# Optimization experiments

Hardware: AMD Instinct MI355X
Metric: run time of the kernel (lower is better)

The kernel has to match this reference:

```python
import jax, jax.numpy as jnp
import numpy as np

U, B, I, D, L = 50000, 20000, 100000, 64, 2
E_UB, E_UI, E_BI = 800000, 1000000, 800000
E_BIAGG, E_UIAGG = 800000, 1000000
UPS_UB = UPS_UI = UPS_BI = 0.1
XI = jnp.array([1.0 / 3, 1.0 / 3, 1.0 / 3], dtype=jnp.float32)  # layer coefs (len L+1)
OMEGA, G1, G2, TAU, LAM1, LAM2 = 0.5, 0.5, 0.5, 0.25, 0.04, 1e-5
BATCH = 2048


def l2norm(x, axis=-1):
    n = jnp.linalg.norm(x, axis=axis, keepdims=True)
    return x / jnp.maximum(n, 1e-12)


def spmm(rows, cols, vals, x, n):
    # sparse [n, m] @ dense [m, D] via gather + segment-sum over COO entries
    return jax.ops.segment_sum(vals[:, None] * x[cols], rows, num_segments=n)


def graph_propagate(rows, cols, vals, A, Bf, noise, ups, xi):
    n = A.shape[0] + Bf.shape[0]
    feats = jnp.concatenate([A, Bf], axis=0)
    alls = [feats]
    for l in range(L):
        feats = spmm(rows, cols, vals, feats, n)
        feats = feats + jnp.sign(feats) * l2norm(noise[l]) * ups  # noise injection
        alls.append(l2norm(feats, axis=1))
    out = jnp.sum(jnp.stack(alls, axis=1) * xi[None, :, None], axis=1)  # weighted layer sum [n, D]
    return out[: A.shape[0]], out[A.shape[0] :]


def graph_aggregate(rows, cols, vals, x, noise, ups, n):
    agg = spmm(rows, cols, vals, x, n)
    return agg + jnp.sign(agg) * l2norm(noise) * ups


def cl_loss(pos, aug):
    pos = l2norm(pos, 1)
    aug = l2norm(aug, 1)
    pos_score = jnp.exp(jnp.sum(pos * aug, axis=1) / TAU)
    ttl = jnp.sum(jnp.exp(pos @ aug.T / TAU), axis=1)
    return -jnp.mean(jnp.log(pos_score / ttl))


def dcbr_forward(users_feature, bundles_feature, items_feature,
                 ub_rows, ub_cols, ub_vals, ui_rows, ui_cols, ui_vals,
                 bi_rows, bi_cols, bi_vals, biagg_rows, biagg_cols, biagg_vals,
                 uiagg_rows, uiagg_cols, uiagg_vals,
                 noise_UB, noise_UI, noise_BI, noise_agg_BI, noise_agg_UI,
                 users, bundles):
    UB_u, UB_b = graph_propagate(ub_rows, ub_cols, ub_vals, users_feature, bundles_feature, noise_UB, UPS_UB, XI)
    UI_u, UI_i = graph_propagate(ui_rows, ui_cols, ui_vals, users_feature, items_feature, noise_UI, UPS_UI, XI)
    UI_b = graph_aggregate(biagg_rows, biagg_cols, biagg_vals, UI_i, noise_agg_BI, UPS_BI, B)
    BI_b, BI_i = graph_propagate(bi_rows, bi_cols, bi_vals, bundles_feature, items_feature, noise_BI, UPS_BI, XI)
    BI_u = graph_aggregate(uiagg_rows, uiagg_cols, uiagg_vals, BI_i, noise_agg_UI, UPS_UI, U)
    users_rep = OMEGA * UI_u + (1 - OMEGA) * BI_u
    bundles_rep = OMEGA * UI_b + (1 - OMEGA) * BI_b
    u_emb = users_rep[users]          # [batch, 1, D] -> broadcasts over negatives
    b_emb = bundles_rep[bundles]      # [batch, 2, D]
    pred = jnp.sum(u_emb * b_emb, axis=2)  # [batch, 2]
    pos, neg = pred[:, :1], pred[:, 1:]
    reg = jnp.sum(users_feature ** 2) + jnp.sum(bundles_feature ** 2) + jnp.sum(items_feature ** 2)
    bpr = -jnp.mean(jax.nn.log_sigmoid(pos - neg)) + LAM2 * reg
    u0, b0 = users[:, 0], bundles[:, 0]
    ub_u, ui_us, bi_us = UB_u[u0], UI_u[u0], BI_u[u0]
    ub_bb, ui_bb, bi_bb = UB_b[b0], UI_b[b0], BI_b[b0]
    u_inter = cl_loss(ub_u, ui_us) + cl_loss(ub_u, bi_us) + cl_loss(ui_us, bi_us)
    b_inter = cl_loss(ub_bb, ui_bb) + cl_loss(ub_bb, bi_bb) + cl_loss(ui_bb, bi_bb)
    u_intra = cl_loss(ub_u, ub_u) + cl_loss(ui_us, ui_us) + cl_loss(bi_us, bi_us)
    b_intra = cl_loss(ub_bb, ub_bb) + cl_loss(ui_bb, ui_bb) + cl_loss(bi_bb, bi_bb)
    cl = LAM1 * (G1 * (u_inter + b_inter) + G2 * (u_intra + b_intra))
    return bpr, cl


def setup_inputs():
    key = jax.random.key(0)
    k = jax.random.split(key, 16)

    def prop_edges(kk, nA, nB, e):
        k1, k2, k3 = jax.random.split(kk, 3)
        a = jax.random.randint(k1, (e,), 0, nA, dtype=jnp.int32)
        b = jax.random.randint(k2, (e,), 0, nB, dtype=jnp.int32) + nA
        v = jax.random.uniform(k3, (e,), jnp.float32, 0.01, 0.2)  # degree-normalized weights
        return jnp.concatenate([a, b]), jnp.concatenate([b, a]), jnp.concatenate([v, v])

    def agg_edges(kk, nA, nB, e):
        k1, k2, k3 = jax.random.split(kk, 3)
        return (jax.random.randint(k1, (e,), 0, nA, dtype=jnp.int32),
                jax.random.randint(k2, (e,), 0, nB, dtype=jnp.int32),
                jax.random.uniform(k3, (e,), jnp.float32, 0.01, 0.2))

    ub_rows, ub_cols, ub_vals = prop_edges(k[0], U, B, E_UB)
    ui_rows, ui_cols, ui_vals = prop_edges(k[1], U, I, E_UI)
    bi_rows, bi_cols, bi_vals = prop_edges(k[2], B, I, E_BI)
    biagg_rows, biagg_cols, biagg_vals = agg_edges(k[3], B, I, E_BIAGG)
    uiagg_rows, uiagg_cols, uiagg_vals = agg_edges(k[4], U, I, E_UIAGG)
    s = 0.02  # xavier-normal-ish scale
    return {
        'users_feature': jax.random.normal(k[5], (U, D), jnp.float32) * s,
        'bundles_feature': jax.random.normal(k[6], (B, D), jnp.float32) * s,
        'items_feature': jax.random.normal(k[7], (I, D), jnp.float32) * s,
        'ub_rows': ub_rows, 'ub_cols': ub_cols, 'ub_vals': ub_vals,
        'ui_rows': ui_rows, 'ui_cols': ui_cols, 'ui_vals': ui_vals,
        'bi_rows': bi_rows, 'bi_cols': bi_cols, 'bi_vals': bi_vals,
        'biagg_rows': biagg_rows, 'biagg_cols': biagg_cols, 'biagg_vals': biagg_vals,
        'uiagg_rows': uiagg_rows, 'uiagg_cols': uiagg_cols, 'uiagg_vals': uiagg_vals,
        'noise_UB': jax.random.uniform(k[8], (L, U + B, D), jnp.float32),
        'noise_UI': jax.random.uniform(k[9], (L, U + I, D), jnp.float32),
        'noise_BI': jax.random.uniform(k[10], (L, B + I, D), jnp.float32),
        'noise_agg_BI': jax.random.uniform(k[11], (B, D), jnp.float32),
        'noise_agg_UI': jax.random.uniform(k[12], (U, D), jnp.float32),
        'users': jax.random.randint(k[13], (BATCH, 1), 0, U, dtype=jnp.int32),
        'bundles': jax.random.randint(k[14], (BATCH, 2), 0, B, dtype=jnp.int32),
    }


def reference(users_feature, bundles_feature, items_feature,
              ub_rows, ub_cols, ub_vals, ui_rows, ui_cols, ui_vals,
              bi_rows, bi_cols, bi_vals, biagg_rows, biagg_cols, biagg_vals,
              uiagg_rows, uiagg_cols, uiagg_vals,
              noise_UB, noise_UI, noise_BI, noise_agg_BI, noise_agg_UI,
              users, bundles):
    return dcbr_forward(users_feature, bundles_feature, items_feature,
                        ub_rows, ub_cols, ub_vals, ui_rows, ui_cols, ui_vals,
                        bi_rows, bi_cols, bi_vals, biagg_rows, biagg_cols, biagg_vals,
                        uiagg_rows, uiagg_cols, uiagg_vals,
                        noise_UB, noise_UI, noise_BI, noise_agg_BI, noise_agg_UI,
                        users, bundles)
```

## Files before the change

### kernel.cpp

```cpp
#include <hip/hip_runtime.h>
#include <cmath>
#include <climits>

#define DD 64

namespace {

constexpr int U_N = 50000, B_N = 20000, I_N = 100000;
constexpr int BATCH = 2048;

constexpr int N1 = 340000, N2 = 70000;
constexpr int SHIFT1 = 10, SHIFT2 = 8;
constexpr int NB1 = (N1 + (1 << SHIFT1) - 1) >> SHIFT1;
constexpr int NB2 = (N2 + (1 << SHIFT2) - 1) >> SHIFT2;

typedef __attribute__((ext_vector_type(8))) short short8;
typedef __attribute__((ext_vector_type(4))) float floatx4;
typedef __attribute__((ext_vector_type(2))) float f32x2;

__device__ __forceinline__ float wave_sum(float v) {
#pragma unroll
  for (int off = 32; off > 0; off >>= 1) v += __shfl_xor(v, off);
  return v;
}

__device__ __forceinline__ float wave_sum16(float v) {
#pragma unroll
  for (int off = 1; off < 16; off <<= 1) v += __shfl_xor(v, off);
  return v;
}

__device__ __forceinline__ unsigned short f2bf(float f) {
  unsigned u = __float_as_uint(f);
  unsigned r = (u + 0x7FFFu + ((u >> 16) & 1u)) >> 16;
  return (unsigned short)r;
}

__device__ __forceinline__ float sgn(float x) {
  return (x > 0.f) ? 1.f : ((x < 0.f) ? -1.f : 0.f);
}

__global__ void k_tobf16(const float* __restrict__ x, unsigned short* __restrict__ o, int n4) {
  int i = blockIdx.x * 256 + threadIdx.x;
  if (i >= n4) return;
  float4 v = ((const float4*)x)[i];
  uint2 p;
  p.x = (unsigned)f2bf(v.x) | ((unsigned)f2bf(v.y) << 16);
  p.y = (unsigned)f2bf(v.z) | ((unsigned)f2bf(v.w) << 16);
  ((uint2*)o)[i] = p;
}

__global__ __launch_bounds__(512) void k_bhist(const int* __restrict__ rows, int nnz,
                                               int row_off, int shift,
                                               const unsigned char* __restrict__ flags,
                                               int* __restrict__ bcnt) {
  __shared__ int h[512];
  int t = threadIdx.x;
  h[t] = 0;
  __syncthreads();
  int tile0 = blockIdx.x * 8192;
#pragma unroll
  for (int i = 0; i < 16; ++i) {
    int e = tile0 + i * 512 + t;
    if (e < nnz) {
      int r = rows[e] + row_off;
      if (!flags || flags[r]) atomicAdd(&h[r >> shift], 1);
    }
  }
  __syncthreads();
  if (h[t]) atomicAdd(&bcnt[t], h[t]);
}

__global__ void k_bucket_scan(const int* __restrict__ bcnt, int nb, int* __restrict__ bbase,
                              int* __restrict__ bcur, int* __restrict__ rowptr_end) {
  int t = threadIdx.x;
  int lane = t & 63, w = t >> 6;
  int v = (t < nb) ? bcnt[t] : 0;
  int inc = v;
#pragma unroll
  for (int off = 1; off < 64; off <<= 1) {
    int y = __shfl_up(inc, off);
    if (lane >= off) inc += y;
  }
  __shared__ int wsum[8];
  if (lane == 63) wsum[w] = inc;
  __syncthreads();
  int wadd = 0;
  for (int i = 0; i < w; ++i) wadd += wsum[i];
  inc += wadd;
  if (t < nb) { bbase[t] = inc - v; bcur[t] = inc - v; }
  if (t == 511) { bbase[nb] = inc; *rowptr_end = inc; }
}

__global__ __launch_bounds__(512) void k_binscatter(const int* __restrict__ rows,
                                                    const int* __restrict__ cols,
                                                    const float* __restrict__ vals, int nnz,
                                                    int row_off, int shift,
                                                    int nAth, int offA, int offB,
                                                    const unsigned char* __restrict__ flags,
                                                    int* __restrict__ bcur,
                                                    int2* __restrict__ ebin_cv) {
  __shared__ int cnt[512];
  __shared__ int gbase[512];
  int t = threadIdx.x;
  int tile0 = blockIdx.x * 8192;
  cnt[t] = 0;
  __syncthreads();
  int r[16], rank[16];
#pragma unroll
  for (int i = 0; i < 16; ++i) {
    int e = tile0 + i * 512 + t;
    rank[i] = -1;
    if (e < nnz) {
      r[i] = rows[e] + row_off;
      if (!flags || flags[r[i]]) rank[i] = atomicAdd(&cnt[r[i] >> shift], 1);
    }
  }
  __syncthreads();
  int c = cnt[t];
  if (c > 0) gbase[t] = atomicAdd(&bcur[t], c);
  __syncthreads();
  int mask = (1 << shift) - 1;
#pragma unroll
  for (int i = 0; i < 16; ++i) {
    int e = tile0 + i * 512 + t;
    if (rank[i] >= 0) {
      int pos = gbase[r[i] >> shift] + rank[i];
      int col = cols[e];
      int gcol = (col < nAth) ? col + offA : col + offB;
      ebin_cv[pos] = make_int2(((r[i] & mask) << 20) | gcol, __float_as_int(vals[e]));
    }
  }
}

__global__ __launch_bounds__(1024) void k_place(const int* __restrict__ bbase, int shift,
                                                int nrows, const int2* __restrict__ ebin_cv,
                                                int* __restrict__ rowptr,
                                                int2* __restrict__ epack) {
  int b = blockIdx.x;
  int bsize = 1 << shift;
  int row0 = b << shift;
  int t = threadIdx.x;
  __shared__ int rcnt[1024];
  __shared__ int wsum[16];
  int ebase = bbase[b], eend = bbase[b + 1];
  if (t < bsize) rcnt[t] = 0;
  __syncthreads();
  for (int e = ebase + t; e < eend; e += 1024)
    atomicAdd(&rcnt[ebin_cv[e].x >> 20], 1);
  __syncthreads();
  int v = (t < bsize) ? rcnt[t] : 0;
  int inc = v;
  int lane = t & 63, w = t >> 6;
#pragma unroll
  for (int off = 1; off < 64; off <<= 1) {
    int y = __shfl_up(inc, off);
    if (lane >= off) inc += y;
  }
  if (lane == 63) wsum[w] = inc;
  __syncthreads();
  int wadd = 0;
  for (int i = 0; i < w; ++i) wadd += wsum[i];
  inc += wadd;
  int excl = inc - v;
  int nr = nrows - row0;
  if (nr > bsize) nr = bsize;
  if (t < nr) rowptr[row0 + t] = ebase + excl;
  __syncthreads();
  if (t < bsize) rcnt[t] = excl;
  __syncthreads();
  for (int e = ebase + t; e < eend; e += 1024) {
    int2 cv = ebin_cv[e];
    int pos = ebase + atomicAdd(&rcnt[cv.x >> 20], 1);
    epack[pos] = make_int2(cv.x & 0xFFFFF, cv.y);
  }
}

__global__ void k_spmm1(const int* __restrict__ rowptr, const int2* __restrict__ epack,
                        const uint2* __restrict__ xg, const float* __restrict__ noise,
                        uint2* __restrict__ s2g, int n, int nAth, int offA, int offB) {
  long long t = (long long)blockIdx.x * 256 + threadIdx.x;
  int row = (int)(t >> 6), lane = (int)(t & 63);
  if (row >= n) return;
  int q = lane >> 4, c = lane & 15;
  unsigned cb = (unsigned)c << 3;
  int s = rowptr[row], e = rowptr[row + 1];
  int em1 = e - 1;
  f32x2 a0[4], a1[4];
#pragma unroll
  for (int j = 0; j < 4; ++j) { a0[j] = (f32x2){0.f, 0.f}; a1[j] = (f32x2){0.f, 0.f}; }
  for (int kk = s; kk < e; kk += 16) {
#pragma unroll
    for (int j = 0; j < 4; ++j) {
      int i = kk + 4 * j + q;
      int ic = min(i, em1);
      int2 ed = epack[ic];
      float v = (i <= em1) ? __int_as_float(ed.y) : 0.f;
      uint2 d = *(const uint2*)((const char*)xg + (((unsigned)ed.x << 7) | cb));
      f32x2 lo = {__uint_as_float(d.x << 16), __uint_as_float(d.x & 0xffff0000u)};
      f32x2 hi = {__uint_as_float(d.y << 16), __uint_as_float(d.y & 0xffff0000u)};
      f32x2 vv = {v, v};
      a0[j] = __builtin_elementwise_fma(lo, vv, a0[j]);
      a1[j] = __builtin_elementwise_fma(hi, vv, a1[j]);
    }
  }
  f32x2 g0 = (a0[0] + a0[1]) + (a0[2] + a0[3]);
  f32x2 g1 = (a1[0] + a1[1]) + (a1[2] + a1[3]);
  float4 g = {g0.x, g0.y, g1.x, g1.y};
  g.x += __shfl_xor(g.x, 16); g.y += __shfl_xor(g.y, 16);
  g.z += __shfl_xor(g.z, 16); g.w += __shfl_xor(g.w, 16);
  g.x += __shfl_xor(g.x, 32); g.y += __shfl_xor(g.y, 32);
  g.z += __shfl_xor(g.z, 32); g.w += __shfl_xor(g.w, 32);
  float4 nz = ((const float4*)(noise + (size_t)row * DD))[c];
  float nn = wave_sum16(nz.x * nz.x + nz.y * nz.y + nz.z * nz.z + nz.w * nz.w) * 0.25f;
  float nf = 0.1f / fmaxf(sqrtf(nn), 1e-12f);
  if (lane < 16) {
    float4 fv;
    fv.x = g.x + sgn(g.x) * nz.x * nf;
    fv.y = g.y + sgn(g.y) * nz.y * nf;
    fv.z = g.z + sgn(g.z) * nz.z * nf;
    fv.w = g.w + sgn(g.w) * nz.w * nf;
    uint2 o;
    o.x = (unsigned)f2bf(fv.x) | ((unsigned)f2bf(fv.y) << 16);
    o.y = (unsigned)f2bf(fv.z) | ((unsigned)f2bf(fv.w) << 16);
    int grow = (row < nAth) ? row + offA : row + offB;
    s2g[grow * 16 + c] = o;
  }
}

__global__ void k_spmm2(const int* __restrict__ rowptr, const int2* __restrict__ epack,
                        const uint2* __restrict__ s2g, const uint2* __restrict__ xg,
                        const float* __restrict__ noise, float* __restrict__ outp,
                        const int* __restrict__ ids, int row_add, int row0, int nw,
                        int nAth, int offA, int offB) {
  long long t = (long long)blockIdx.x * 256 + threadIdx.x;
  int w = (int)(t >> 6), lane = (int)(t & 63);
  if (w >= nw) return;
  int row = ids ? (ids[w] + row_add) : (row0 + w);
  int q = lane >> 4, c = lane & 15;
  unsigned cb = (unsigned)c << 3;
  int s = rowptr[row], e = rowptr[row + 1];
  int em1 = e - 1;
  f32x2 a0[4], a1[4];
#pragma unroll
  for (int j = 0; j < 4; ++j) { a0[j] = (f32x2){0.f, 0.f}; a1[j] = (f32x2){0.f, 0.f}; }
  for (int kk = s; kk < e; kk += 16) {
#pragma unroll
    for (int j = 0; j < 4; ++j) {
      int i = kk + 4 * j + q;
      int ic = min(i, em1);
      int2 ed = epack[ic];
      float v = (i <= em1) ? __int_as_float(ed.y) : 0.f;
      uint2 d = *(const uint2*)((const char*)s2g + (((unsigned)ed.x << 7) | cb));
      f32x2 lo = {__uint_as_float(d.x << 16), __uint_as_float(d.x & 0xffff0000u)};
      f32x2 hi = {__uint_as_float(d.y << 16), __uint_as_float(d.y & 0xffff0000u)};
      f32x2 vv = {v, v};
      a0[j] = __builtin_elementwise_fma(lo, vv, a0[j]);
      a1[j] = __builtin_elementwise_fma(hi, vv, a1[j]);
    }
  }
  f32x2 g0 = (a0[0] + a0[1]) + (a0[2] + a0[3]);
  f32x2 g1 = (a1[0] + a1[1]) + (a1[2] + a1[3]);
  float4 g = {g0.x, g0.y, g1.x, g1.y};
  g.x += __shfl_xor(g.x, 16); g.y += __shfl_xor(g.y, 16);
  g.z += __shfl_xor(g.z, 16); g.w += __shfl_xor(g.w, 16);
  g.x += __shfl_xor(g.x, 32); g.y += __shfl_xor(g.y, 32);
  g.z += __shfl_xor(g.z, 32); g.w += __shfl_xor(g.w, 32);
  float4 nz = ((const float4*)(noise + (size_t)row * DD))[c];
  float nn = wave_sum16(nz.x * nz.x + nz.y * nz.y + nz.z * nz.z + nz.w * nz.w) * 0.25f;
  float nf = 0.1f / fmaxf(sqrtf(nn), 1e-12f);
  float4 fv;
  fv.x = g.x + sgn(g.x) * nz.x * nf;
  fv.y = g.y + sgn(g.y) * nz.y * nf;
  fv.z = g.z + sgn(g.z) * nz.z * nf;
  fv.w = g.w + sgn(g.w) * nz.w * nf;
  float fn2 = wave_sum16(fv.x * fv.x + fv.y * fv.y + fv.z * fv.z + fv.w * fv.w) * 0.25f;
  float inv2 = (1.f / 3.f) / fmaxf(sqrtf(fn2), 1e-12f);
  int grow = (row < nAth) ? row + offA : row + offB;
  uint2 s1p = s2g[grow * 16 + c];
  float4 s1;
  s1.x = __uint_as_float(s1p.x << 16);
  s1.y = __uint_as_float(s1p.x & 0xffff0000u);
  s1.z = __uint_as_float(s1p.y << 16);
  s1.w = __uint_as_float(s1p.y & 0xffff0000u);
  float fn1 = wave_sum16(s1.x * s1.x + s1.y * s1.y + s1.z * s1.z + s1.w * s1.w) * 0.25f;
  float inv1 = (1.f / 3.f) / fmaxf(sqrtf(fn1), 1e-12f);
  uint2 x0p = xg[grow * 16 + c];
  float4 x0;
  x0.x = __uint_as_float(x0p.x << 16);
  x0.y = __uint_as_float(x0p.x & 0xffff0000u);
  x0.z = __uint_as_float(x0p.y << 16);
  x0.w = __uint_as_float(x0p.y & 0xffff0000u);
  if (lane < 16) {
    float4 o;
    o.x = x0.x * (1.f / 3.f) + s1.x * inv1 + fv.x * inv2;
    o.y = x0.y * (1.f / 3.f) + s1.y * inv1 + fv.y * inv2;
    o.z = x0.z * (1.f / 3.f) + s1.z * inv1 + fv.z * inv2;
    o.w = x0.w * (1.f / 3.f) + s1.w * inv1 + fv.w * inv2;
    ((float4*)(outp + (size_t)w * DD))[c] = o;
  }
}

__global__ void k_agg_s(const int* __restrict__ rowptr, const int2* __restrict__ epack,
                        const float* __restrict__ x, const float* __restrict__ noise,
                        const int* __restrict__ ids, int nids, float* __restrict__ out) {
  long long t = (long long)blockIdx.x * 256 + threadIdx.x;
  int w = (int)(t >> 6), lane = (int)(t & 63);
  if (w >= nids) return;
  int row = ids[w];
  int q = lane >> 4, c = lane & 15;
  int s = rowptr[row], e = rowptr[row + 1];
  int em1 = e - 1;
  float4 a0 = {0.f, 0.f, 0.f, 0.f}, a1 = {0.f, 0.f, 0.f, 0.f};
  for (int kk = s; kk < e; kk += 8) {
    int i0 = kk + q, i1 = kk + 4 + q;
    int2 e0 = epack[min(i0, em1)];
    int2 e1 = epack[min(i1, em1)];
    float4 x0 = ((const float4*)(x + (size_t)e0.x * DD))[c];
    float4 x1 = ((const float4*)(x + (size_t)e1.x * DD))[c];
    float v0 = (i0 <= em1) ? __int_as_float(e0.y) : 0.f;
    float v1 = (i1 <= em1) ? __int_as_float(e1.y) : 0.f;
    a0.x = fmaf(v0, x0.x, a0.x); a0.y = fmaf(v0, x0.y, a0.y);
    a0.z = fmaf(v0, x0.z, a0.z); a0.w = fmaf(v0, x0.w, a0.w);
    a1.x = fmaf(v1, x1.x, a1.x); a1.y = fmaf(v1, x1.y, a1.y);
    a1.z = fmaf(v1, x1.z, a1.z); a1.w = fmaf(v1, x1.w, a1.w);
  }
  float4 g;
  g.x = a0.x + a1.x; g.y = a0.y + a1.y; g.z = a0.z + a1.z; g.w = a0.w + a1.w;
  g.x += __shfl_xor(g.x, 16); g.y += __shfl_xor(g.y, 16);
  g.z += __shfl_xor(g.z, 16); g.w += __shfl_xor(g.w, 16);
  g.x += __shfl_xor(g.x, 32); g.y += __shfl_xor(g.y, 32);
  g.z += __shfl_xor(g.z, 32); g.w += __shfl_xor(g.w, 32);
  float4 nz = ((const float4*)(noise + (size_t)row * DD))[c];
  float nn = wave_sum16(nz.x * nz.x + nz.y * nz.y + nz.z * nz.z + nz.w * nz.w) * 0.25f;
  float nf = 0.1f / fmaxf(sqrtf(nn), 1e-12f);
  if (lane < 16) {
    float4 fv;
    fv.x = g.x + sgn(g.x) * nz.x * nf;
    fv.y = g.y + sgn(g.y) * nz.y * nf;
    fv.z = g.z + sgn(g.z) * nz.z * nf;
    fv.w = g.w + sgn(g.w) * nz.w * nf;
    ((float4*)(out + (size_t)w * DD))[c] = fv;
  }
}

__global__ void k_flag(const int* __restrict__ users, const int* __restrict__ bundles,
                       unsigned char* __restrict__ flags) {
  int t = blockIdx.x * 256 + threadIdx.x;
  if (t < BATCH) flags[20000 + users[t]] = 1;
  if (t < 2 * BATCH) flags[bundles[t]] = 1;
}

__global__ void k_bpr(const float* __restrict__ o_UIuS, const float* __restrict__ biuS,
                      const float* __restrict__ uibS, const float* __restrict__ o_BIbS,
                      float* __restrict__ bpr_terms) {
  long long t = (long long)blockIdx.x * 256 + threadIdx.x;
  int w = (int)(t >> 6);
  int lane = (int)(t & 63);
  if (w >= BATCH) return;
  float ur = 0.5f * (o_UIuS[(size_t)w * DD + lane] + biuS[(size_t)w * DD + lane]);
  float br0 = 0.5f * (uibS[(size_t)(2 * w) * DD + lane] + o_BIbS[(size_t)(2 * w) * DD + lane]);
  float br1 = 0.5f * (uibS[(size_t)(2 * w + 1) * DD + lane] +
                      o_BIbS[(size_t)(2 * w + 1) * DD + lane]);
  float pos = wave_sum(ur * br0);
  float neg = wave_sum(ur * br1);
  if (lane == 0) {
    float x = pos - neg;
    float loss = (x > 0.f) ? log1pf(expf(-x)) : (-x + log1pf(expf(x)));
    bpr_terms[w] = loss;
  }
}

__global__ void k_sumsq_p(const float* __restrict__ x, int n4, float* __restrict__ partials) {
  float s = 0.f;
  for (int i = blockIdx.x * 256 + threadIdx.x; i < n4; i += gridDim.x * 256) {
    float4 v = ((const float4*)x)[i];
    s += v.x * v.x + v.y * v.y + v.z * v.z + v.w * v.w;
  }
  s = wave_sum(s);
  __shared__ float part[4];
  if ((threadIdx.x & 63) == 0) part[threadIdx.x >> 6] = s;
  __syncthreads();
  if (threadIdx.x == 0) partials[blockIdx.x] = part[0] + part[1] + part[2] + part[3];
}

__global__ void k_gather(const float* __restrict__ o_UBS, const float* __restrict__ o_UIuS,
                         const float* __restrict__ o_BIbS, const float* __restrict__ uibS,
                         const float* __restrict__ biuS, float* __restrict__ P,
                         unsigned short* __restrict__ Pb) {
  long long t = (long long)blockIdx.x * 256 + threadIdx.x;
  int w = (int)(t >> 6);
  int lane = (int)(t & 63);
  if (w >= 6 * BATCH) return;
  int k = w / BATCH, b = w % BATCH;
  const float* src;
  if (k == 0)      src = o_UBS + (size_t)b * DD;
  else if (k == 1) src = o_UIuS + (size_t)b * DD;
  else if (k == 2) src = biuS + (size_t)b * DD;
  else if (k == 3) src = o_UBS + (size_t)(2048 + 2 * b) * DD;
  else if (k == 4) src = uibS + (size_t)(2 * b) * DD;
  else             src = o_BIbS + (size_t)(2 * b) * DD;
  float v = src[lane];
  float n2 = wave_sum(v * v);
  float inv = 1.f / fmaxf(sqrtf(n2), 1e-12f);
  float pv = v * inv;
  P[(size_t)w * DD + lane] = pv;
  Pb[(size_t)w * DD + lane] = f2bf(pv);
}

__global__ void k_clpair_mfma(const unsigned short* __restrict__ Pb,
                              float* __restrict__ ttl) {
  const int pairX[12] = {0, 0, 1, 0, 1, 2, 3, 3, 4, 3, 4, 5};
  const int pairY[12] = {1, 2, 2, 0, 1, 2, 4, 5, 5, 3, 4, 5};
  int wid = threadIdx.x >> 6;
  int lane = threadIdx.x & 63;
  int wtile = blockIdx.x * 4 + wid;
  int p = wtile >> 8;
  int rest = wtile & 255;
  int it = rest >> 3, jc = rest & 7;
  const unsigned short* X = Pb + (size_t)pairX[p] * BATCH * DD;
  const unsigned short* Y = Pb + (size_t)pairY[p] * BATCH * DD;
  int r = lane & 15, q = lane >> 4;
  short8 A[2][4];
#pragma unroll
  for (int kh = 0; kh < 2; ++kh)
#pragma unroll
    for (int ii = 0; ii < 4; ++ii)
      A[kh][ii] = *(const short8*)(X + (size_t)(it * 64 + ii * 16 + r) * DD + kh * 32 + q * 8);
  float rs[4][4];
#pragma unroll
  for (int ii = 0; ii < 4; ++ii)
#pragma unroll
    for (int g = 0; g < 4; ++g) rs[ii][g] = 0.f;
  for (int jn = 0; jn < 4; ++jn) {
    int j0 = jc * 256 + jn * 64;
    floatx4 acc[4][4];
#pragma unroll
    for (int ii = 0; ii < 4; ++ii)
#pragma unroll
      for (int jj = 0; jj < 4; ++jj) acc[ii][jj] = (floatx4){0.f, 0.f, 0.f, 0.f};
#pragma unroll
    for (int kh = 0; kh < 2; ++kh) {
      short8 Bf[4];
#pragma unroll
      for (int jj = 0; jj < 4; ++jj)
        Bf[jj] = *(const short8*)(Y + (size_t)(j0 + jj * 16 + r) * DD + kh * 32 + q * 8);
#pragma unroll
      for (int ii = 0; ii < 4; ++ii)
#pragma unroll
        for (int jj = 0; jj < 4; ++jj)
          acc[ii][jj] = __builtin_amdgcn_mfma_f32_16x16x32_bf16(A[kh][ii], Bf[jj],
                                                                acc[ii][jj], 0, 0, 0);
    }
#pragma unroll
    for (int ii = 0; ii < 4; ++ii)
#pragma unroll
      for (int jj = 0; jj < 4; ++jj)
#pragma unroll
        for (int g = 0; g < 4; ++g) rs[ii][g] += __expf(4.0f * acc[ii][jj][g]);
  }
#pragma unroll
  for (int off = 1; off < 16; off <<= 1)
#pragma unroll
    for (int ii = 0; ii < 4; ++ii)
#pragma unroll
      for (int g = 0; g < 4; ++g) rs[ii][g] += __shfl_xor(rs[ii][g], off);
  if (r == 0) {
#pragma unroll
    for (int ii = 0; ii < 4; ++ii)
#pragma unroll
      for (int g = 0; g < 4; ++g)
        unsafeAtomicAdd(&ttl[(size_t)p * BATCH + it * 64 + ii * 16 + q * 4 + g],
                        rs[ii][g]);
  }
}

__global__ void k_cldiag(const float* __restrict__ P, float* __restrict__ ttl) {
  const int pairX[12] = {0, 0, 1, 0, 1, 2, 3, 3, 4, 3, 4, 5};
  const int pairY[12] = {1, 2, 2, 0, 1, 2, 4, 5, 5, 3, 4, 5};
  long long t = (long long)blockIdx.x * 256 + threadIdx.x;
  int w = (int)(t >> 6);
  int lane = (int)(t & 63);
  if (w >= 12 * BATCH) return;
  int p = w / BATCH, i = w % BATCH;
  float xv = P[((size_t)pairX[p] * BATCH + i) * DD + lane];
  float yv = P[((size_t)pairY[p] * BATCH + i) * DD + lane];
  float d = wave_sum(xv * yv);
  if (lane == 0) ttl[(size_t)p * BATCH + i] = logf(ttl[(size_t)p * BATCH + i]) - d * 4.0f;
}

__global__ void k_finalred(const float* __restrict__ bpr_terms,
                           const float* __restrict__ cl_terms,
                           const float* __restrict__ partials,
                           float* __restrict__ out) {
  int t = threadIdx.x;
  float bpr = 0.f, reg = 0.f, inter = 0.f, intra = 0.f;
  for (int i = t; i < BATCH; i += 1024) bpr += bpr_terms[i];
  for (int i = t; i < 768; i += 1024) reg += partials[i];
  for (int i = t; i < 12 * BATCH; i += 1024) {
    int p = i >> 11;
    float v = cl_terms[i];
    if ((p % 6) < 3) inter += v; else intra += v;
  }
  bpr = wave_sum(bpr); reg = wave_sum(reg);
  inter = wave_sum(inter); intra = wave_sum(intra);
  __shared__ float sb[16], sr[16], si[16], sx[16];
  int w = t >> 6, lane = t & 63;
  if (lane == 0) { sb[w] = bpr; sr[w] = reg; si[w] = inter; sx[w] = intra; }
  __syncthreads();
  if (t == 0) {
    float Bs = 0, Rs = 0, Is = 0, Xs = 0;
    for (int i = 0; i < 16; ++i) { Bs += sb[i]; Rs += sr[i]; Is += si[i]; Xs += sx[i]; }
    out[0] = Bs / (float)BATCH + 1e-5f * Rs;
    out[1] = 0.04f * (0.5f * Is + 0.5f * Xs) / (float)BATCH;
  }
}

}

extern "C" void kernel_launch(void* const* d_in, const int* in_sizes, int n_in,
                              void* d_out, int out_size, void* d_ws, size_t ws_size,
                              hipStream_t stream) {
  const float* usersF = (const float*)d_in[0];
  const float* bundlesF = (const float*)d_in[1];
  const float* itemsF = (const float*)d_in[2];
  const int* ub_rows = (const int*)d_in[3];
  const int* ub_cols = (const int*)d_in[4];
  const float* ub_vals = (const float*)d_in[5];
  const int* ui_rows = (const int*)d_in[6];
  const int* ui_cols = (const int*)d_in[7];
  const float* ui_vals = (const float*)d_in[8];
  const int* bi_rows = (const int*)d_in[9];
  const int* bi_cols = (const int*)d_in[10];
  const float* bi_vals = (const float*)d_in[11];
  const int* biagg_rows = (const int*)d_in[12];
  const int* biagg_cols = (const int*)d_in[13];
  const float* biagg_vals = (const float*)d_in[14];
  const int* uiagg_rows = (const int*)d_in[15];
  const int* uiagg_cols = (const int*)d_in[16];
  const float* uiagg_vals = (const float*)d_in[17];
  const float* noise_UB = (const float*)d_in[18];
  const float* noise_UI = (const float*)d_in[19];
  const float* noise_BI = (const float*)d_in[20];
  const float* noise_agg_BI = (const float*)d_in[21];
  const float* noise_agg_UI = (const float*)d_in[22];
  const int* users = (const int*)d_in[23];
  const int* bundles = (const int*)d_in[24];
  int nnz_ub = in_sizes[3], nnz_ui = in_sizes[6], nnz_bi = in_sizes[9];
  int nnz_biagg = in_sizes[12], nnz_uiagg = in_sizes[15];

  float* ws = (float*)d_ws;
  size_t off = 0;
  float* o_UBS  = ws + off; off += (size_t)(3 * BATCH) * DD;
  float* o_UIuS = ws + off; off += (size_t)BATCH * DD;
  float* o_UIit = ws + off; off += (size_t)I_N * DD;
  float* o_BIbS = ws + off; off += (size_t)(2 * BATCH) * DD;
  float* o_BIit = ws + off; off += (size_t)I_N * DD;
  float* uibS = ws + off; off += (size_t)2 * BATCH * DD;
  float* biuS = ws + off; off += (size_t)BATCH * DD;
  unsigned short* s2g16 = (unsigned short*)(ws + off); off += (size_t)170000 * DD / 2;
  unsigned short* xb16  = (unsigned short*)(ws + off); off += (size_t)170000 * DD / 2;
  float* P    = ws + off; off += (size_t)6 * BATCH * DD;
  float* ttl  = ws + off; off += (size_t)12 * BATCH;
  float* bprT = ws + off; off += BATCH;
  float* prt  = ws + off; off += 768;
  int* rptr  = (int*)(ws + off); off += N1 + 1;
  int* bcnt  = (int*)(ws + off); off += 512;
  int* bbase = (int*)(ws + off); off += 520;
  int* bcur  = (int*)(ws + off); off += 512;
  unsigned char* flags = (unsigned char*)(ws + off); off += 17500;
  off = (off + 1) & ~(size_t)1;
  int2* epack = (int2*)(ws + off); off += (size_t)5200000 * 2;
  if (ws_size < off * sizeof(float)) return;

  unsigned short* Pb = (unsigned short*)s2g16;
  int2* ebin_cv1 = (int2*)ws;
  int2* ebin_cv2 = (int2*)s2g16;

  const uint2* xgv = (const uint2*)xb16;
  uint2* s2gv = (uint2*)s2g16;

  auto gb = [](int nnz) { return (nnz + 8191) / 8192; };

  k_tobf16<<<(U_N * 16 + 255) / 256, 256, 0, stream>>>(usersF, xb16, U_N * 16);
  k_tobf16<<<(B_N * 16 + 255) / 256, 256, 0, stream>>>(bundlesF, xb16 + (size_t)U_N * DD,
                                                       B_N * 16);
  k_tobf16<<<(I_N * 16 + 255) / 256, 256, 0, stream>>>(itemsF, xb16 + (size_t)(U_N + B_N) * DD,
                                                       I_N * 16);

  int* rp_ub = rptr, * rp_ui = rptr + 70000, * rp_bi = rptr + 220000;
  hipMemsetAsync(bcnt, 0, 512 * sizeof(int), stream);
  k_bhist<<<gb(nnz_ub), 512, 0, stream>>>(ub_rows, nnz_ub, 0, SHIFT1, nullptr, bcnt);
  k_bhist<<<gb(nnz_ui), 512, 0, stream>>>(ui_rows, nnz_ui, 70000, SHIFT1, nullptr, bcnt);
  k_bhist<<<gb(nnz_bi), 512, 0, stream>>>(bi_rows, nnz_bi, 220000, SHIFT1, nullptr, bcnt);
  k_bucket_scan<<<1, 512, 0, stream>>>(bcnt, NB1, bbase, bcur, rptr + N1);
  k_binscatter<<<gb(nnz_ub), 512, 0, stream>>>(ub_rows, ub_cols, ub_vals, nnz_ub, 0, SHIFT1,
                                               INT_MAX, 0, 0, nullptr, bcur, ebin_cv1);
  k_binscatter<<<gb(nnz_ui), 512, 0, stream>>>(ui_rows, ui_cols, ui_vals, nnz_ui, 70000, SHIFT1,
                                               50000, 0, 20000, nullptr, bcur, ebin_cv1);
  k_binscatter<<<gb(nnz_bi), 512, 0, stream>>>(bi_rows, bi_cols, bi_vals, nnz_bi, 220000, SHIFT1,
                                               0, 50000, 50000, nullptr, bcur, ebin_cv1);
  k_place<<<NB1, 1024, 0, stream>>>(bbase, SHIFT1, N1, ebin_cv1, rptr, epack);

  {
    int n = 70000;
    k_spmm1<<<(int)(((long long)n * 64 + 255) / 256), 256, 0, stream>>>(
        rp_ub, epack, xgv, noise_UB, s2gv, n, INT_MAX, 0, 0);
    const float* nz2 = noise_UB + (size_t)n * DD;
    k_spmm2<<<BATCH * 64 / 256, 256, 0, stream>>>(rp_ub, epack, s2gv, xgv, nz2, o_UBS,
                                                  users, 0, 0, BATCH, INT_MAX, 0, 0);
    k_spmm2<<<2 * BATCH * 64 / 256, 256, 0, stream>>>(rp_ub, epack, s2gv, xgv, nz2,
                                                      o_UBS + (size_t)2048 * DD,
                                                      bundles, 50000, 0, 2 * BATCH,
                                                      INT_MAX, 0, 0);
  }
  {
    int n = 150000;
    k_spmm1<<<(int)(((long long)n * 64 + 255) / 256), 256, 0, stream>>>(
        rp_ui, epack, xgv, noise_UI, s2gv, n, 50000, 0, 20000);
    const float* nz2 = noise_UI + (size_t)n * DD;
    k_spmm2<<<BATCH * 64 / 256, 256, 0, stream>>>(rp_ui, epack, s2gv, xgv, nz2, o_UIuS,
                                                  users, 0, 0, BATCH, 50000, 0, 20000);
    k_spmm2<<<(int)(((long long)I_N * 64 + 255) / 256), 256, 0, stream>>>(
        rp_ui, epack, s2gv, xgv, nz2, o_UIit, nullptr, 0, 50000, I_N, 50000, 0, 20000);
  }
  {
    int n = 120000;
    k_spmm1<<<(int)(((long long)n * 64 + 255) / 256), 256, 0, stream>>>(
        rp_bi, epack, xgv, noise_BI, s2gv, n, 0, 50000, 50000);
    const float* nz2 = noise_BI + (size_t)n * DD;
    k_spmm2<<<2 * BATCH * 64 / 256, 256, 0, stream>>>(rp_bi, epack, s2gv, xgv, nz2, o_BIbS,
                                                      bundles, 0, 0, 2 * BATCH, 0, 50000,
                                                      50000);
    k_spmm2<<<(int)(((long long)I_N * 64 + 255) / 256), 256, 0, stream>>>(
        rp_bi, epack, s2gv, xgv, nz2, o_BIit, nullptr, 0, 20000, I_N, 0, 50000, 50000);
  }

  int* rp_ba = rptr, * rp_ua = rptr + 20000;
  hipMemsetAsync(flags, 0, 70000, stream);
  k_flag<<<(2 * BATCH + 255) / 256, 256, 0, stream>>>(users, bundles, flags);
  hipMemsetAsync(bcnt, 0, 512 * sizeof(int), stream);
  k_bhist<<<gb(nnz_biagg), 512, 0, stream>>>(biagg_rows, nnz_biagg, 0, SHIFT2, flags, bcnt);
  k_bhist<<<gb(nnz_uiagg), 512, 0, stream>>>(uiagg_rows, nnz_uiagg, 20000, SHIFT2, flags, bcnt);
  k_bucket_scan<<<1, 512, 0, stream>>>(bcnt, NB2, bbase, bcur, rptr + N2);
  k_binscatter<<<gb(nnz_biagg), 512, 0, stream>>>(biagg_rows, biagg_cols, biagg_vals, nnz_biagg,
                                                  0, SHIFT2, INT_MAX, 0, 0, flags, bcur,
                                                  ebin_cv2);
  k_binscatter<<<gb(nnz_uiagg), 512, 0, stream>>>(uiagg_rows, uiagg_cols, uiagg_vals, nnz_uiagg,
                                                  20000, SHIFT2, INT_MAX, 0, 0, flags, bcur,
                                                  ebin_cv2);
  k_place<<<NB2, 1024, 0, stream>>>(bbase, SHIFT2, N2, ebin_cv2, rptr, epack);

  k_agg_s<<<(2 * BATCH * 64) / 256, 256, 0, stream>>>(
      rp_ba, epack, o_UIit, noise_agg_BI, bundles, 2 * BATCH, uibS);
  k_agg_s<<<(BATCH * 64) / 256, 256, 0, stream>>>(
      rp_ua, epack, o_BIit, noise_agg_UI, users, BATCH, biuS);

  k_bpr<<<BATCH * 64 / 256, 256, 0, stream>>>(o_UIuS, biuS, uibS, o_BIbS, bprT);
  k_sumsq_p<<<256, 256, 0, stream>>>(usersF, U_N * DD / 4, prt);
  k_sumsq_p<<<256, 256, 0, stream>>>(bundlesF, B_N * DD / 4, prt + 256);
  k_sumsq_p<<<256, 256, 0, stream>>>(itemsF, I_N * DD / 4, prt + 512);
  k_gather<<<6 * BATCH * 64 / 256, 256, 0, stream>>>(o_UBS, o_UIuS, o_BIbS, uibS, biuS,
                                                     P, Pb);
  hipMemsetAsync(ttl, 0, (size_t)12 * BATCH * sizeof(float), stream);
  k_clpair_mfma<<<768, 256, 0, stream>>>(Pb, ttl);
  k_cldiag<<<12 * BATCH * 64 / 256, 256, 0, stream>>>(P, ttl);
  k_finalred<<<1, 1024, 0, stream>>>(bprT, ttl, prt, (float*)d_out);
}
```

Measured before the change: 998.1 us.

## Merge per-graph SpMM launches into fused kernels with two rows per wave

The three graphs' first-layer SpMMs become one launch, and the second-layer item and sampled-row SpMMs each become one launch, using separate bf16 intermediate buffers per graph so they no longer serialize on a shared buffer. Each 64-lane wave now processes two rows (32 lanes each) instead of one, halving idle lanes on short rows. Edge and noise loads use nontemporal hints, and the two aggregation launches are merged into one. This cuts launch count and underutilization, but needs more workspace and gives less edge parallelism per row.

```diff
diff --git a/kernel.cpp b/kernel.cpp
--- a/kernel.cpp
+++ b/kernel.cpp
@@ -17,6 +17,8 @@
 typedef __attribute__((ext_vector_type(8))) short short8;
 typedef __attribute__((ext_vector_type(4))) float floatx4;
 typedef __attribute__((ext_vector_type(2))) float f32x2;
+typedef __attribute__((ext_vector_type(4))) float f4v;
+typedef __attribute__((ext_vector_type(2))) int i2v;
 
 __device__ __forceinline__ float wave_sum(float v) {
 #pragma unroll
@@ -176,27 +178,20 @@
   }
 }
 
-__global__ void k_spmm1(const int* __restrict__ rowptr, const int2* __restrict__ epack,
-                        const uint2* __restrict__ xg, const float* __restrict__ noise,
-                        uint2* __restrict__ s2g, int n, int nAth, int offA, int offB) {
-  long long t = (long long)blockIdx.x * 256 + threadIdx.x;
-  int row = (int)(t >> 6), lane = (int)(t & 63);
-  if (row >= n) return;
-  int q = lane >> 4, c = lane & 15;
-  unsigned cb = (unsigned)c << 3;
-  int s = rowptr[row], e = rowptr[row + 1];
+__device__ __forceinline__ float4 gather_row_bf16(int s, int e, int q, unsigned cb,
+                                                  const int2* __restrict__ epack,
+                                                  const uint2* __restrict__ src) {
   int em1 = e - 1;
   f32x2 a0[4], a1[4];
 #pragma unroll
   for (int j = 0; j < 4; ++j) { a0[j] = (f32x2){0.f, 0.f}; a1[j] = (f32x2){0.f, 0.f}; }
-  for (int kk = s; kk < e; kk += 16) {
+  for (int kk = s; kk < e; kk += 8) {
 #pragma unroll
     for (int j = 0; j < 4; ++j) {
-      int i = kk + 4 * j + q;
-      int ic = min(i, em1);
-      int2 ed = epack[ic];
+      int i = kk + 2 * j + q;
+      i2v ed = __builtin_nontemporal_load((const i2v*)epack + min(i, em1));
       float v = (i <= em1) ? __int_as_float(ed.y) : 0.f;
-      uint2 d = *(const uint2*)((const char*)xg + (((unsigned)ed.x << 7) | cb));
+      uint2 d = *(const uint2*)((const char*)src + (((unsigned)ed.x << 7) | cb));
       f32x2 lo = {__uint_as_float(d.x << 16), __uint_as_float(d.x & 0xffff0000u)};
       f32x2 hi = {__uint_as_float(d.y << 16), __uint_as_float(d.y & 0xffff0000u)};
       f32x2 vv = {v, v};
@@ -209,12 +204,41 @@
   float4 g = {g0.x, g0.y, g1.x, g1.y};
   g.x += __shfl_xor(g.x, 16); g.y += __shfl_xor(g.y, 16);
   g.z += __shfl_xor(g.z, 16); g.w += __shfl_xor(g.w, 16);
-  g.x += __shfl_xor(g.x, 32); g.y += __shfl_xor(g.y, 32);
-  g.z += __shfl_xor(g.z, 32); g.w += __shfl_xor(g.w, 32);
-  float4 nz = ((const float4*)(noise + (size_t)row * DD))[c];
+  return g;
+}
+
+__global__ __launch_bounds__(256) void k_spmm1_all(
+    const int* __restrict__ rowptr, const int2* __restrict__ epack,
+    const uint2* __restrict__ xg, const float* __restrict__ nzUB,
+    const float* __restrict__ nzUI, const float* __restrict__ nzBI,
+    uint2* __restrict__ s2ub, uint2* __restrict__ s2ui, uint2* __restrict__ s2bi_adj) {
+  long long t = (long long)blockIdx.x * 256 + threadIdx.x;
+  int wv = (int)(t >> 6), lane = (int)(t & 63);
+  if (wv >= 170000) return;
+  int h = lane >> 5, q = (lane >> 4) & 1, c = lane & 15;
+  unsigned cb = (unsigned)c << 3;
+  int row = 2 * wv + h;
+  const float* nrow;
+  uint2* s2row;
+  if (row < 70000) {
+    nrow = nzUB + (size_t)row * DD;
+    s2row = s2ub + (size_t)row * 16;
+  } else if (row < 220000) {
+    int lr = row - 70000;
+    nrow = nzUI + (size_t)lr * DD;
+    int node = (lr < 50000) ? lr : lr + 20000;
+    s2row = s2ui + (size_t)node * 16;
+  } else {
+    int lr = row - 220000;
+    nrow = nzBI + (size_t)lr * DD;
+    s2row = s2bi_adj + (size_t)(lr + 50000) * 16;
+  }
+  int s = rowptr[row], e = rowptr[row + 1];
+  float4 g = gather_row_bf16(s, e, q, cb, epack, xg);
+  f4v nz = __builtin_nontemporal_load((const f4v*)nrow + c);
   float nn = wave_sum16(nz.x * nz.x + nz.y * nz.y + nz.z * nz.z + nz.w * nz.w) * 0.25f;
   float nf = 0.1f / fmaxf(sqrtf(nn), 1e-12f);
-  if (lane < 16) {
+  if (q == 0) {
     float4 fv;
     fv.x = g.x + sgn(g.x) * nz.x * nf;
     fv.y = g.y + sgn(g.y) * nz.y * nf;
@@ -223,50 +247,18 @@
     uint2 o;
     o.x = (unsigned)f2bf(fv.x) | ((unsigned)f2bf(fv.y) << 16);
     o.y = (unsigned)f2bf(fv.z) | ((unsigned)f2bf(fv.w) << 16);
-    int grow = (row < nAth) ? row + offA : row + offB;
-    s2g[grow * 16 + c] = o;
-  }
-}
-
-__global__ void k_spmm2(const int* __restrict__ rowptr, const int2* __restrict__ epack,
-                        const uint2* __restrict__ s2g, const uint2* __restrict__ xg,
-                        const float* __restrict__ noise, float* __restrict__ outp,
-                        const int* __restrict__ ids, int row_add, int row0, int nw,
-                        int nAth, int offA, int offB) {
-  long long t = (long long)blockIdx.x * 256 + threadIdx.x;
-  int w = (int)(t >> 6), lane = (int)(t & 63);
-  if (w >= nw) return;
-  int row = ids ? (ids[w] + row_add) : (row0 + w);
-  int q = lane >> 4, c = lane & 15;
-  unsigned cb = (unsigned)c << 3;
-  int s = rowptr[row], e = rowptr[row + 1];
-  int em1 = e - 1;
-  f32x2 a0[4], a1[4];
-#pragma unroll
-  for (int j = 0; j < 4; ++j) { a0[j] = (f32x2){0.f, 0.f}; a1[j] = (f32x2){0.f, 0.f}; }
-  for (int kk = s; kk < e; kk += 16) {
-#pragma unroll
-    for (int j = 0; j < 4; ++j) {
-      int i = kk + 4 * j + q;
-      int ic = min(i, em1);
-      int2 ed = epack[ic];
-      float v = (i <= em1) ? __int_as_float(ed.y) : 0.f;
-      uint2 d = *(const uint2*)((const char*)s2g + (((unsigned)ed.x << 7) | cb));
-      f32x2 lo = {__uint_as_float(d.x << 16), __uint_as_float(d.x & 0xffff0000u)};
-      f32x2 hi = {__uint_as_float(d.y << 16), __uint_as_float(d.y & 0xffff0000u)};
-      f32x2 vv = {v, v};
-      a0[j] = __builtin_elementwise_fma(lo, vv, a0[j]);
-      a1[j] = __builtin_elementwise_fma(hi, vv, a1[j]);
-    }
-  }
-  f32x2 g0 = (a0[0] + a0[1]) + (a0[2] + a0[3]);
-  f32x2 g1 = (a1[0] + a1[1]) + (a1[2] + a1[3]);
-  float4 g = {g0.x, g0.y, g1.x, g1.y};
-  g.x += __shfl_xor(g.x, 16); g.y += __shfl_xor(g.y, 16);
-  g.z += __shfl_xor(g.z, 16); g.w += __shfl_xor(g.w, 16);
-  g.x += __shfl_xor(g.x, 32); g.y += __shfl_xor(g.y, 32);
-  g.z += __shfl_xor(g.z, 32); g.w += __shfl_xor(g.w, 32);
-  float4 nz = ((const float4*)(noise + (size_t)row * DD))[c];
+    s2row[c] = o;
+  }
+}
+
+__device__ __forceinline__ void spmm2_body(int s, int e, int q, int c, unsigned cb,
+                                           const int2* __restrict__ epack,
+                                           const uint2* __restrict__ s2,
+                                           const uint2* __restrict__ xg, int node,
+                                           const float* __restrict__ nrow,
+                                           float* __restrict__ orow) {
+  float4 g = gather_row_bf16(s, e, q, cb, epack, s2);
+  f4v nz = __builtin_nontemporal_load((const f4v*)nrow + c);
   float nn = wave_sum16(nz.x * nz.x + nz.y * nz.y + nz.z * nz.z + nz.w * nz.w) * 0.25f;
   float nf = 0.1f / fmaxf(sqrtf(nn), 1e-12f);
   float4 fv;
@@ -276,8 +268,7 @@
   fv.w = g.w + sgn(g.w) * nz.w * nf;
   float fn2 = wave_sum16(fv.x * fv.x + fv.y * fv.y + fv.z * fv.z + fv.w * fv.w) * 0.25f;
   float inv2 = (1.f / 3.f) / fmaxf(sqrtf(fn2), 1e-12f);
-  int grow = (row < nAth) ? row + offA : row + offB;
-  uint2 s1p = s2g[grow * 16 + c];
+  uint2 s1p = s2[(size_t)node * 16 + c];
   float4 s1;
   s1.x = __uint_as_float(s1p.x << 16);
   s1.y = __uint_as_float(s1p.x & 0xffff0000u);
@@ -285,62 +276,162 @@
   s1.w = __uint_as_float(s1p.y & 0xffff0000u);
   float fn1 = wave_sum16(s1.x * s1.x + s1.y * s1.y + s1.z * s1.z + s1.w * s1.w) * 0.25f;
   float inv1 = (1.f / 3.f) / fmaxf(sqrtf(fn1), 1e-12f);
-  uint2 x0p = xg[grow * 16 + c];
+  uint2 x0p = xg[(size_t)node * 16 + c];
   float4 x0;
   x0.x = __uint_as_float(x0p.x << 16);
   x0.y = __uint_as_float(x0p.x & 0xffff0000u);
   x0.z = __uint_as_float(x0p.y << 16);
   x0.w = __uint_as_float(x0p.y & 0xffff0000u);
-  if (lane < 16) {
+  if (q == 0) {
     float4 o;
     o.x = x0.x * (1.f / 3.f) + s1.x * inv1 + fv.x * inv2;
     o.y = x0.y * (1.f / 3.f) + s1.y * inv1 + fv.y * inv2;
     o.z = x0.z * (1.f / 3.f) + s1.z * inv1 + fv.z * inv2;
     o.w = x0.w * (1.f / 3.f) + s1.w * inv1 + fv.w * inv2;
-    ((float4*)(outp + (size_t)w * DD))[c] = o;
-  }
-}
-
-__global__ void k_agg_s(const int* __restrict__ rowptr, const int2* __restrict__ epack,
-                        const float* __restrict__ x, const float* __restrict__ noise,
-                        const int* __restrict__ ids, int nids, float* __restrict__ out) {
+    ((float4*)orow)[c] = o;
+  }
+}
+
+__global__ __launch_bounds__(256) void k_spmm2_items(
+    const int* __restrict__ rowptr, const int2* __restrict__ epack,
+    const uint2* __restrict__ xg, const uint2* __restrict__ s2ui,
+    const uint2* __restrict__ s2bi_adj, const float* __restrict__ nzUI,
+    const float* __restrict__ nzBI, float* __restrict__ o_UIit,
+    float* __restrict__ o_BIit) {
   long long t = (long long)blockIdx.x * 256 + threadIdx.x;
-  int w = (int)(t >> 6), lane = (int)(t & 63);
-  if (w >= nids) return;
-  int row = ids[w];
-  int q = lane >> 4, c = lane & 15;
-  int s = rowptr[row], e = rowptr[row + 1];
+  int wv = (int)(t >> 6), lane = (int)(t & 63);
+  if (wv >= 100000) return;
+  int h = lane >> 5, q = (lane >> 4) & 1, c = lane & 15;
+  unsigned cb = (unsigned)c << 3;
+  const uint2* s2;
+  const float* nrow;
+  float* orow;
+  int grow, node;
+  if (wv < 50000) {
+    int ii = 2 * wv + h;
+    grow = 120000 + ii;
+    node = 70000 + ii;
+    s2 = s2ui;
+    nrow = nzUI + (size_t)(200000 + ii) * DD;
+    orow = o_UIit + (size_t)ii * DD;
+  } else {
+    int ii = 2 * (wv - 50000) + h;
+    grow = 240000 + ii;
+    node = 70000 + ii;
+    s2 = s2bi_adj;
+    nrow = nzBI + (size_t)(140000 + ii) * DD;
+    orow = o_BIit + (size_t)ii * DD;
+  }
+  int s = rowptr[grow], e = rowptr[grow + 1];
+  spmm2_body(s, e, q, c, cb, epack, s2, xg, node, nrow, orow);
+}
+
+__global__ __launch_bounds__(256) void k_spmm2_samp(
+    const int* __restrict__ rowptr, const int2* __restrict__ epack,
+    const uint2* __restrict__ xg, const uint2* __restrict__ s2ub,
+    const uint2* __restrict__ s2ui, const uint2* __restrict__ s2bi_adj,
+    const float* __restrict__ nzUB, const float* __restrict__ nzUI,
+    const float* __restrict__ nzBI, const int* __restrict__ users,
+    const int* __restrict__ bundles, float* __restrict__ o_UBS,
+    float* __restrict__ o_UIuS, float* __restrict__ o_BIbS) {
+  long long t = (long long)blockIdx.x * 256 + threadIdx.x;
+  int wv = (int)(t >> 6), lane = (int)(t & 63);
+  if (wv >= 6144) return;
+  int h = lane >> 5, q = (lane >> 4) & 1, c = lane & 15;
+  unsigned cb = (unsigned)c << 3;
+  const uint2* s2;
+  const float* nrow;
+  float* orow;
+  int grow, node;
+  if (wv < 1024) {
+    int ii = 2 * wv + h;
+    int id = users[ii];
+    grow = id; node = id; s2 = s2ub;
+    nrow = nzUB + (size_t)(70000 + id) * DD;
+    orow = o_UBS + (size_t)ii * DD;
+  } else if (wv < 3072) {
+    int ii = 2 * (wv - 1024) + h;
+    int id = bundles[ii];
+    node = 50000 + id; grow = node; s2 = s2ub;
+    nrow = nzUB + (size_t)(70000 + node) * DD;
+    orow = o_UBS + (size_t)(2048 + ii) * DD;
+  } else if (wv < 4096) {
+    int ii = 2 * (wv - 3072) + h;
+    int id = users[ii];
+    grow = 70000 + id; node = id; s2 = s2ui;
+    nrow = nzUI + (size_t)(150000 + id) * DD;
+    orow = o_UIuS + (size_t)ii * DD;
+  } else {
+    int ii = 2 * (wv - 4096) + h;
+    int id = bundles[ii];
+    grow = 220000 + id; node = 50000 + id; s2 = s2bi_adj;
+    nrow = nzBI + (size_t)(120000 + id) * DD;
+    orow = o_BIbS + (size_t)ii * DD;
+  }
+  int s = rowptr[grow], e = rowptr[grow + 1];
+  spmm2_body(s, e, q, c, cb, epack, s2, xg, node, nrow, orow);
+}
+
+__global__ __launch_bounds__(256) void k_agg2(
+    const int* __restrict__ rowptr, const int2* __restrict__ epack,
+    const float* __restrict__ o_UIit, const float* __restrict__ o_BIit,
+    const float* __restrict__ nzBA, const float* __restrict__ nzUA,
+    const int* __restrict__ users, const int* __restrict__ bundles,
+    float* __restrict__ uibS, float* __restrict__ biuS) {
+  long long t = (long long)blockIdx.x * 256 + threadIdx.x;
+  int wv = (int)(t >> 6), lane = (int)(t & 63);
+  if (wv >= 3072) return;
+  int h = lane >> 5, q = (lane >> 4) & 1, c = lane & 15;
+  const float* x;
+  const float* nrow;
+  float* orow;
+  int grow;
+  if (wv < 2048) {
+    int ii = 2 * wv + h;
+    int id = bundles[ii];
+    grow = id; x = o_UIit;
+    nrow = nzBA + (size_t)id * DD;
+    orow = uibS + (size_t)ii * DD;
+  } else {
+    int ii = 2 * (wv - 2048) + h;
+    int id = users[ii];
+    grow = 20000 + id; x = o_BIit;
+    nrow = nzUA + (size_t)id * DD;
+    orow = biuS + (size_t)ii * DD;
+  }
+  int s = rowptr[grow], e = rowptr[grow + 1];
   int em1 = e - 1;
-  float4 a0 = {0.f, 0.f, 0.f, 0.f}, a1 = {0.f, 0.f, 0.f, 0.f};
+  float4 a[4];
+#pragma unroll
+  for (int j = 0; j < 4; ++j) a[j] = (float4){0.f, 0.f, 0.f, 0.f};
   for (int kk = s; kk < e; kk += 8) {
-    int i0 = kk + q, i1 = kk + 4 + q;
-    int2 e0 = epack[min(i0, em1)];
-    int2 e1 = epack[min(i1, em1)];
-    float4 x0 = ((const float4*)(x + (size_t)e0.x * DD))[c];
-    float4 x1 = ((const float4*)(x + (size_t)e1.x * DD))[c];
-    float v0 = (i0 <= em1) ? __int_as_float(e0.y) : 0.f;
-    float v1 = (i1 <= em1) ? __int_as_float(e1.y) : 0.f;
-    a0.x = fmaf(v0, x0.x, a0.x); a0.y = fmaf(v0, x0.y, a0.y);
-    a0.z = fmaf(v0, x0.z, a0.z); a0.w = fmaf(v0, x0.w, a0.w);
-    a1.x = fmaf(v1, x1.x, a1.x); a1.y = fmaf(v1, x1.y, a1.y);
-    a1.z = fmaf(v1, x1.z, a1.z); a1.w = fmaf(v1, x1.w, a1.w);
+#pragma unroll
+    for (int j = 0; j < 4; ++j) {
+      int i = kk + 2 * j + q;
+      i2v ed = __builtin_nontemporal_load((const i2v*)epack + min(i, em1));
+      float v = (i <= em1) ? __int_as_float(ed.y) : 0.f;
+      float4 xv = ((const float4*)(x + (size_t)ed.x * DD))[c];
+      a[j].x = fmaf(v, xv.x, a[j].x); a[j].y = fmaf(v, xv.y, a[j].y);
+      a[j].z = fmaf(v, xv.z, a[j].z); a[j].w = fmaf(v, xv.w, a[j].w);
+    }
   }
   float4 g;
-  g.x = a0.x + a1.x; g.y = a0.y + a1.y; g.z = a0.z + a1.z; g.w = a0.w + a1.w;
+  g.x = (a[0].x + a[1].x) + (a[2].x + a[3].x);
+  g.y = (a[0].y + a[1].y) + (a[2].y + a[3].y);
+  g.z = (a[0].z + a[1].z) + (a[2].z + a[3].z);
+  g.w = (a[0].w + a[1].w) + (a[2].w + a[3].w);
   g.x += __shfl_xor(g.x, 16); g.y += __shfl_xor(g.y, 16);
   g.z += __shfl_xor(g.z, 16); g.w += __shfl_xor(g.w, 16);
-  g.x += __shfl_xor(g.x, 32); g.y += __shfl_xor(g.y, 32);
-  g.z += __shfl_xor(g.z, 32); g.w += __shfl_xor(g.w, 32);
-  float4 nz = ((const float4*)(noise + (size_t)row * DD))[c];
+  f4v nz = __builtin_nontemporal_load((const f4v*)nrow + c);
   float nn = wave_sum16(nz.x * nz.x + nz.y * nz.y + nz.z * nz.z + nz.w * nz.w) * 0.25f;
   float nf = 0.1f / fmaxf(sqrtf(nn), 1e-12f);
-  if (lane < 16) {
+  if (q == 0) {
     float4 fv;
     fv.x = g.x + sgn(g.x) * nz.x * nf;
     fv.y = g.y + sgn(g.y) * nz.y * nf;
     fv.z = g.z + sgn(g.z) * nz.z * nf;
     fv.w = g.w + sgn(g.w) * nz.w * nf;
-    ((float4*)(out + (size_t)w * DD))[c] = fv;
+    ((float4*)orow)[c] = fv;
   }
 }
 
@@ -558,8 +649,10 @@
   float* o_BIit = ws + off; off += (size_t)I_N * DD;
   float* uibS = ws + off; off += (size_t)2 * BATCH * DD;
   float* biuS = ws + off; off += (size_t)BATCH * DD;
-  unsigned short* s2g16 = (unsigned short*)(ws + off); off += (size_t)170000 * DD / 2;
-  unsigned short* xb16  = (unsigned short*)(ws + off); off += (size_t)170000 * DD / 2;
+  unsigned short* s2ub16 = (unsigned short*)(ws + off); off += (size_t)70000 * DD / 2;
+  unsigned short* s2ui16 = (unsigned short*)(ws + off); off += (size_t)170000 * DD / 2;
+  unsigned short* s2bi16 = (unsigned short*)(ws + off); off += (size_t)120000 * DD / 2;
+  unsigned short* xb16   = (unsigned short*)(ws + off); off += (size_t)170000 * DD / 2;
   float* P    = ws + off; off += (size_t)6 * BATCH * DD;
   float* ttl  = ws + off; off += (size_t)12 * BATCH;
   float* bprT = ws + off; off += BATCH;
@@ -573,12 +666,14 @@
   int2* epack = (int2*)(ws + off); off += (size_t)5200000 * 2;
   if (ws_size < off * sizeof(float)) return;
 
-  unsigned short* Pb = (unsigned short*)s2g16;
   int2* ebin_cv1 = (int2*)ws;
-  int2* ebin_cv2 = (int2*)s2g16;
+  int2* ebin_cv2 = (int2*)s2ui16;
+  unsigned short* Pb = s2ub16;
 
   const uint2* xgv = (const uint2*)xb16;
-  uint2* s2gv = (uint2*)s2g16;
+  uint2* s2ub = (uint2*)s2ub16;
+  uint2* s2ui = (uint2*)s2ui16;
+  uint2* s2bi_adj = (uint2*)s2bi16 - (size_t)50000 * 16;
 
   auto gb = [](int nnz) { return (nnz + 8191) / 8192; };
 
@@ -588,7 +683,6 @@
   k_tobf16<<<(I_N * 16 + 255) / 256, 256, 0, stream>>>(itemsF, xb16 + (size_t)(U_N + B_N) * DD,
                                                        I_N * 16);
 
-  int* rp_ub = rptr, * rp_ui = rptr + 70000, * rp_bi = rptr + 220000;
   hipMemsetAsync(bcnt, 0, 512 * sizeof(int), stream);
   k_bhist<<<gb(nnz_ub), 512, 0, stream>>>(ub_rows, nnz_ub, 0, SHIFT1, nullptr, bcnt);
   k_bhist<<<gb(nnz_ui), 512, 0, stream>>>(ui_rows, nnz_ui, 70000, SHIFT1, nullptr, bcnt);
@@ -602,41 +696,14 @@
                                                0, 50000, 50000, nullptr, bcur, ebin_cv1);
   k_place<<<NB1, 1024, 0, stream>>>(bbase, SHIFT1, N1, ebin_cv1, rptr, epack);
 
-  {
-    int n = 70000;
-    k_spmm1<<<(int)(((long long)n * 64 + 255) / 256), 256, 0, stream>>>(
-        rp_ub, epack, xgv, noise_UB, s2gv, n, INT_MAX, 0, 0);
-    const float* nz2 = noise_UB + (size_t)n * DD;
-    k_spmm2<<<BATCH * 64 / 256, 256, 0, stream>>>(rp_ub, epack, s2gv, xgv, nz2, o_UBS,
-                                                  users, 0, 0, BATCH, INT_MAX, 0, 0);
-    k_spmm2<<<2 * BATCH * 64 / 256, 256, 0, stream>>>(rp_ub, epack, s2gv, xgv, nz2,
-                                                      o_UBS + (size_t)2048 * DD,
-                                                      bundles, 50000, 0, 2 * BATCH,
-                                                      INT_MAX, 0, 0);
-  }
-  {
-    int n = 150000;
-    k_spmm1<<<(int)(((long long)n * 64 + 255) / 256), 256, 0, stream>>>(
-        rp_ui, epack, xgv, noise_UI, s2gv, n, 50000, 0, 20000);
-    const float* nz2 = noise_UI + (size_t)n * DD;
-    k_spmm2<<<BATCH * 64 / 256, 256, 0, stream>>>(rp_ui, epack, s2gv, xgv, nz2, o_UIuS,
-                                                  users, 0, 0, BATCH, 50000, 0, 20000);
-    k_spmm2<<<(int)(((long long)I_N * 64 + 255) / 256), 256, 0, stream>>>(
-        rp_ui, epack, s2gv, xgv, nz2, o_UIit, nullptr, 0, 50000, I_N, 50000, 0, 20000);
-  }
-  {
-    int n = 120000;
-    k_spmm1<<<(int)(((long long)n * 64 + 255) / 256), 256, 0, stream>>>(
-        rp_bi, epack, xgv, noise_BI, s2gv, n, 0, 50000, 50000);
-    const float* nz2 = noise_BI + (size_t)n * DD;
-    k_spmm2<<<2 * BATCH * 64 / 256, 256, 0, stream>>>(rp_bi, epack, s2gv, xgv, nz2, o_BIbS,
-                                                      bundles, 0, 0, 2 * BATCH, 0, 50000,
-                                                      50000);
-    k_spmm2<<<(int)(((long long)I_N * 64 + 255) / 256), 256, 0, stream>>>(
-        rp_bi, epack, s2gv, xgv, nz2, o_BIit, nullptr, 0, 20000, I_N, 0, 50000, 50000);
-  }
-
-  int* rp_ba = rptr, * rp_ua = rptr + 20000;
+  k_spmm1_all<<<42500, 256, 0, stream>>>(rptr, epack, xgv, noise_UB, noise_UI, noise_BI,
+                                         s2ub, s2ui, s2bi_adj);
+  k_spmm2_items<<<25000, 256, 0, stream>>>(rptr, epack, xgv, s2ui, s2bi_adj,
+                                           noise_UI, noise_BI, o_UIit, o_BIit);
+  k_spmm2_samp<<<1536, 256, 0, stream>>>(rptr, epack, xgv, s2ub, s2ui, s2bi_adj,
+                                         noise_UB, noise_UI, noise_BI, users, bundles,
+                                         o_UBS, o_UIuS, o_BIbS);
+
   hipMemsetAsync(flags, 0, 70000, stream);
   k_flag<<<(2 * BATCH + 255) / 256, 256, 0, stream>>>(users, bundles, flags);
   hipMemsetAsync(bcnt, 0, 512 * sizeof(int), stream);
@@ -651,10 +718,8 @@
                                                   ebin_cv2);
   k_place<<<NB2, 1024, 0, stream>>>(bbase, SHIFT2, N2, ebin_cv2, rptr, epack);
 
-  k_agg_s<<<(2 * BATCH * 64) / 256, 256, 0, stream>>>(
-      rp_ba, epack, o_UIit, noise_agg_BI, bundles, 2 * BATCH, uibS);
-  k_agg_s<<<(BATCH * 64) / 256, 256, 0, stream>>>(
-      rp_ua, epack, o_BIit, noise_agg_UI, users, BATCH, biuS);
+  k_agg2<<<768, 256, 0, stream>>>(rptr, epack, o_UIit, o_BIit, noise_agg_BI, noise_agg_UI,
+                                  users, bundles, uibS, biuS);
 
   k_bpr<<<BATCH * 64 / 256, 256, 0, stream>>>(o_UIuS, biuS, uibS, o_BIbS, bprT);
   k_sumsq_p<<<256, 256, 0, stream>>>(usersF, U_N * DD / 4, prt);
```

Result: faster. 862.9 us (-13.5%).
